# Kernel tuning notes

Hardware: AMD Instinct MI355X
Metric: run time of the kernel (lower is better)

The kernel has to match this reference:

```python
import jax, jax.numpy as jnp
import numpy as np

K_TOP = 8
TEMP = 1.0
GUMBEL_EPS = 1e-20
GEN_EPS = 1e-7
NEG_INF = -1e9


def _genconv(xn, src, dst, e, We, be, W1, b1, W2, b2):
    """GENConv: edge-proj, m=relu(x_src+e)+eps, per-dst softmax aggregation (t=1),
    residual add, then 2-layer MLP."""
    N = xn.shape[0]
    ep = e @ We + be                         # [E, C]
    m = jax.nn.relu(xn[src] + ep) + GEN_EPS  # [E, C]
    mx = jax.ops.segment_max(m, dst, num_segments=N)
    mx = jnp.where(jnp.isfinite(mx), mx, 0.0)
    w = jnp.exp(m - mx[dst])
    den = jax.ops.segment_sum(w, dst, num_segments=N)
    agg = jax.ops.segment_sum(w * m, dst, num_segments=N) / jnp.where(den > 0, den, 1.0)
    out = agg + xn
    return jax.nn.relu(out @ W1 + b1) @ W2 + b2


def setup_inputs() -> dict:
    key = jax.random.key(0)
    ks = jax.random.split(key, 16)
    N, E, D, ED = 1024, 16384, 128, 16
    H1, H2, OUT = 64, 64, 40
    s = 0.02
    return {
        "x": jax.random.normal(ks[0], (N, D), jnp.float32),
        "edge_attr": jax.random.normal(ks[1], (E, ED), jnp.float32),
        "gumbel_u": jax.random.uniform(ks[2], (N, N), jnp.float32),
        "mlp_w": jax.random.normal(ks[3], (ED + 2 * D, 1), jnp.float32) * s,
        "mlp_b": jnp.zeros((1,), jnp.float32),
        "c1_we": jax.random.normal(ks[4], (ED, D), jnp.float32) * s,
        "c1_be": jnp.zeros((D,), jnp.float32),
        "c1_w1": jax.random.normal(ks[5], (D, 2 * D), jnp.float32) * s,
        "c1_b1": jnp.zeros((2 * D,), jnp.float32),
        "c1_w2": jax.random.normal(ks[6], (2 * D, H1), jnp.float32) * s,
        "c1_b2": jnp.zeros((H1,), jnp.float32),
        "c2_we": jax.random.normal(ks[7], (ED, H1), jnp.float32) * s,
        "c2_be": jnp.zeros((H1,), jnp.float32),
        "c2_w1": jax.random.normal(ks[8], (H1, 2 * H1), jnp.float32) * s,
        "c2_b1": jnp.zeros((2 * H1,), jnp.float32),
        "c2_w2": jax.random.normal(ks[9], (2 * H1, H2), jnp.float32) * s,
        "c2_b2": jnp.zeros((H2,), jnp.float32),
        "fc_w": jax.random.normal(ks[10], (H2, OUT), jnp.float32) * s,
        "fc_b": jnp.zeros((OUT,), jnp.float32),
        "num_nodes": N,
        "edge_index": jax.random.randint(ks[11], (2, E), 0, N),
        "node_mask": jnp.ones((N,), jnp.int32),
    }


def reference(x, edge_attr, gumbel_u, mlp_w, mlp_b,
              c1_we, c1_be, c1_w1, c1_b1, c1_w2, c1_b2,
              c2_we, c2_be, c2_w1, c2_b1, c2_w2, c2_b2,
              fc_w, fc_b, num_nodes, edge_index, node_mask):
    N, D = x.shape
    src, dst = edge_index[0], edge_index[1]

    # dense adjacency (duplicate edges sum, only used as a zero/nonzero mask)
    adj = jnp.zeros((N, N), x.dtype).at[src, dst].add(1.0)

    # Edge-score MLP on concat([x_u, x_v*mask, edge_attr_dense]) decomposed
    # linearly (same math as scoring the dense [N,N,2D+ED] feature tensor).
    w_node, w_nb, w_e = mlp_w[:D], mlp_w[D:2 * D], mlp_w[2 * D:]
    s_edge = jnp.zeros((N, N), x.dtype).at[src, dst].set((edge_attr @ w_e)[:, 0])
    score = (x @ w_node) + (x @ w_nb).T * (adj > 0) + s_edge + mlp_b[0]
    score = jnp.where(adj == 0, NEG_INF, score)

    z = jax.nn.softmax(score, axis=-1)
    g = -jnp.log(-jnp.log(gumbel_u + GUMBEL_EPS) + GUMBEL_EPS)
    z = jax.nn.softmax((z + g) / TEMP, axis=-1)

    # top-k edge sampling; softmax output is strictly positive so valid_mask
    # (z>0) is always all-True and shapes stay static at N*k edges.
    _, topi = jax.lax.top_k(z, K_TOP)                       # [N, k]
    new_src = jnp.repeat(jnp.arange(N), K_TOP)
    new_dst = topi.reshape(-1)

    # match each new edge against old edge list (argmax of boolean equality,
    # unmatched edges fall back to index 0 exactly as torch argmax does)
    eq = (edge_index[0][None, :] == new_src[:, None]) & \
         (edge_index[1][None, :] == new_dst[:, None])       # [N*k, E]
    new_attr = edge_attr[jnp.argmax(eq, axis=-1)]

    h = _genconv(x, new_src, new_dst, new_attr, c1_we, c1_be, c1_w1, c1_b1, c1_w2, c1_b2)
    h = jax.nn.relu(h)
    h = _genconv(h, new_src, new_dst, new_attr, c2_we, c2_be, c2_w1, c2_b1, c2_w2, c2_b2)
    h = jax.nn.relu(h)
    out = h @ fc_w + fc_b
    # node_mask is all ones, so x[node_mask != 0] == identity; masked write
    # keeps static shapes under jit.
    return jnp.where((node_mask != 0)[:, None], out, 0.0)
```

## Files before the change

### kernel.cpp

```cpp
#include <hip/hip_runtime.h>
#include <cfloat>

#define NN   1024
#define NE   16384
#define D0   128
#define EDIM 16
#define NH1  64
#define NOUT 40
#define KTOP 8
#define NEGINF (-1000000000.0f)

#define OFF_IDMAX   0u
#define OFF_IDMIN   4194304u
#define OFF_MX1     8388608u
#define OFF_DEN1    8912896u
#define OFF_NUM1    9437184u
#define OFF_MX2     9961472u
#define OFF_DEN2    10223616u
#define OFF_NUM2    10485760u
#define ZERO_LEN    2359296u
#define OFF_A       10747904u
#define OFF_B       10752000u
#define OFF_DST     10756096u
#define OFF_EM      10788864u
#define OFF_M1      10821632u
#define OFF_OUT1    15015936u
#define OFF_T1      15540224u
#define OFF_H       16588800u
#define OFF_M2      16850944u
#define OFF_OUT2    18948096u
#define OFF_T2      19210240u

__global__ __launch_bounds__(256) void scatter_kernel(
    const int* __restrict__ ei, int* __restrict__ idmax, unsigned* __restrict__ idmin)
{
    int e = blockIdx.x * 256 + threadIdx.x;
    if (e >= NE) return;
    int s = ei[e];
    int d = ei[NE + e];
    int idx = s * NN + d;
    atomicMax(idmax + idx, e);
    atomicMin(idmin + idx, (unsigned)e);
}

__global__ __launch_bounds__(256) void ab_kernel(
    const float* __restrict__ x, const float* __restrict__ mlp_w,
    float* __restrict__ a, float* __restrict__ b)
{
    int i = blockIdx.x * 256 + threadIdx.x;
    if (i >= NN) return;
    const float* xr = x + i * D0;
    float sa = 0.f, sb = 0.f;
    for (int d = 0; d < D0; d++) {
        float xv = xr[d];
        sa += xv * mlp_w[d];
        sb += xv * mlp_w[D0 + d];
    }
    a[i] = sa;
    b[i] = sb;
}

__global__ __launch_bounds__(256) void row_topk_kernel(
    const int* __restrict__ idmax, const unsigned* __restrict__ idmin,
    const float* __restrict__ ea, const float* __restrict__ mlp_w,
    const float* __restrict__ mlp_b, const float* __restrict__ a,
    const float* __restrict__ b, const float* __restrict__ u,
    int* __restrict__ dsti, int* __restrict__ ematch)
{
    __shared__ float sv[NN];
    __shared__ float red_v[256];
    __shared__ int   red_j[256];
    const int i = blockIdx.x;
    const int t = threadIdx.x;
    const int rowoff = i * NN;
    const float bias = mlp_b[0];
    const float ai = a[i];
    float we[EDIM];
    #pragma unroll
    for (int k = 0; k < EDIM; k++) we[k] = mlp_w[2 * D0 + k];

    float lmax = NEGINF;
    for (int j = t; j < NN; j += 256) {
        int id = idmax[rowoff + j];
        float s;
        if (id >= 0) {
            const float* er = ea + id * EDIM;
            float se = 0.f;
            #pragma unroll
            for (int k = 0; k < EDIM; k++) se += er[k] * we[k];
            s = ((ai + b[j]) + se) + bias;
        } else {
            s = NEGINF;
        }
        sv[j] = s;
        lmax = fmaxf(lmax, s);
    }
    red_v[t] = lmax;
    __syncthreads();
    for (int stp = 128; stp > 0; stp >>= 1) {
        if (t < stp) red_v[t] = fmaxf(red_v[t], red_v[t + stp]);
        __syncthreads();
    }
    float rowmax = red_v[0];
    __syncthreads();
    bool noedge = (rowmax == NEGINF);

    float lsum = 0.f;
    for (int j = t; j < NN; j += 256) {
        float e;
        if (noedge) e = 1.0f;
        else {
            float s = sv[j];
            e = (s == NEGINF) ? 0.0f : expf(s - rowmax);
        }
        sv[j] = e;
        lsum += e;
    }
    __syncthreads();
    red_v[t] = lsum;
    __syncthreads();
    for (int stp = 128; stp > 0; stp >>= 1) {
        if (t < stp) red_v[t] += red_v[t + stp];
        __syncthreads();
    }
    float rsum = red_v[0];
    __syncthreads();

    for (int j = t; j < NN; j += 256) {
        float z = sv[j] / rsum;
        float uu = u[rowoff + j];
        float g = -logf(-logf(uu + 1e-20f) + 1e-20f);
        sv[j] = z + g;
    }
    __syncthreads();

    for (int sel = 0; sel < KTOP; sel++) {
        float bv = -FLT_MAX;
        int bj = NN;
        for (int j = t; j < NN; j += 256) {
            float v = sv[j];
            if (v > bv || (v == bv && j < bj)) { bv = v; bj = j; }
        }
        red_v[t] = bv; red_j[t] = bj;
        __syncthreads();
        for (int stp = 128; stp > 0; stp >>= 1) {
            if (t < stp) {
                float ov = red_v[t + stp]; int oj = red_j[t + stp];
                if (ov > red_v[t] || (ov == red_v[t] && oj < red_j[t])) {
                    red_v[t] = ov; red_j[t] = oj;
                }
            }
            __syncthreads();
        }
        if (t == 0) {
            int j = red_j[0];
            dsti[i * KTOP + sel] = j;
            unsigned em = idmin[rowoff + j];
            ematch[i * KTOP + sel] = (em == 0xFFFFFFFFu) ? 0 : (int)em;
            sv[j] = -FLT_MAX;
        }
        __syncthreads();
    }
}

template<int Dd>
__global__ __launch_bounds__(256) void genconv_m_kernel(
    const float* __restrict__ xin, const float* __restrict__ ea,
    const float* __restrict__ we, const float* __restrict__ be,
    const int* __restrict__ ematch, const int* __restrict__ dsti,
    float* __restrict__ m, float* __restrict__ mx)
{
    int gid = blockIdx.x * 256 + threadIdx.x;
    int n = gid / Dd;
    int d = gid % Dd;
    int i = n >> 3;
    int e = ematch[n];
    const float* er = ea + e * EDIM;
    float ep = 0.f;
    #pragma unroll
    for (int k = 0; k < EDIM; k++) ep += er[k] * we[k * Dd + d];
    ep += be[d];
    float v = xin[i * Dd + d] + ep;
    float mm = fmaxf(v, 0.f) + 1e-7f;
    m[n * Dd + d] = mm;
    int dst = dsti[n];
    atomicMax((int*)(mx + dst * Dd + d), __float_as_int(mm));
}

template<int Dd>
__global__ __launch_bounds__(256) void genconv_w_kernel(
    const float* __restrict__ m, const float* __restrict__ mx,
    const int* __restrict__ dsti, float* __restrict__ den, float* __restrict__ num)
{
    int gid = blockIdx.x * 256 + threadIdx.x;
    int n = gid / Dd;
    int d = gid % Dd;
    int dst = dsti[n];
    float mm = m[n * Dd + d];
    float w = expf(mm - mx[dst * Dd + d]);
    atomicAdd(den + dst * Dd + d, w);
    atomicAdd(num + dst * Dd + d, w * mm);
}

template<int Dd>
__global__ __launch_bounds__(256) void genconv_agg_kernel(
    const float* __restrict__ num, const float* __restrict__ den,
    const float* __restrict__ xin, float* __restrict__ out)
{
    int gid = blockIdx.x * 256 + threadIdx.x;
    float dn = den[gid];
    float agg = num[gid] / (dn > 0.f ? dn : 1.f);
    out[gid] = agg + xin[gid];
}

template<int Din, int Dout, bool RELU>
__global__ __launch_bounds__(Dout) void mlp_kernel(
    const float* __restrict__ A, const float* __restrict__ W,
    const float* __restrict__ bias, float* __restrict__ C)
{
    __shared__ float arow[Din];
    int r = blockIdx.x, t = threadIdx.x;
    for (int d = t; d < Din; d += Dout) arow[d] = A[r * Din + d];
    __syncthreads();
    float acc = 0.f;
    for (int d = 0; d < Din; d++) acc += arow[d] * W[d * Dout + t];
    acc += bias[t];
    if (RELU) acc = fmaxf(acc, 0.f);
    C[r * Dout + t] = acc;
}

__global__ __launch_bounds__(64) void final_kernel(
    const float* __restrict__ t2, const float* __restrict__ w2,
    const float* __restrict__ b2, const float* __restrict__ fcw,
    const float* __restrict__ fcb, const int* __restrict__ mask,
    float* __restrict__ out)
{
    __shared__ float arow[2 * NH1];
    __shared__ float h2[NH1];
    int r = blockIdx.x, t = threadIdx.x;
    for (int d = t; d < 2 * NH1; d += 64) arow[d] = t2[r * 2 * NH1 + d];
    __syncthreads();
    float acc = 0.f;
    for (int d = 0; d < 2 * NH1; d++) acc += arow[d] * w2[d * NH1 + t];
    acc += b2[t];
    h2[t] = fmaxf(acc, 0.f);
    __syncthreads();
    if (t < NOUT) {
        float o = 0.f;
        for (int d = 0; d < NH1; d++) o += h2[d] * fcw[d * NOUT + t];
        o += fcb[t];
        out[r * NOUT + t] = (mask[r] != 0) ? o : 0.f;
    }
}

extern "C" void kernel_launch(void* const* d_in, const int* in_sizes, int n_in,
                              void* d_out, int out_size, void* d_ws, size_t ws_size,
                              hipStream_t stream) {
    const float* x      = (const float*)d_in[0];
    const float* ea     = (const float*)d_in[1];
    const float* u      = (const float*)d_in[2];
    const float* mlp_w  = (const float*)d_in[3];
    const float* mlp_b  = (const float*)d_in[4];
    const float* c1_we  = (const float*)d_in[5];
    const float* c1_be  = (const float*)d_in[6];
    const float* c1_w1  = (const float*)d_in[7];
    const float* c1_b1  = (const float*)d_in[8];
    const float* c1_w2  = (const float*)d_in[9];
    const float* c1_b2  = (const float*)d_in[10];
    const float* c2_we  = (const float*)d_in[11];
    const float* c2_be  = (const float*)d_in[12];
    const float* c2_w1  = (const float*)d_in[13];
    const float* c2_b1  = (const float*)d_in[14];
    const float* c2_w2  = (const float*)d_in[15];
    const float* c2_b2  = (const float*)d_in[16];
    const float* fc_w   = (const float*)d_in[17];
    const float* fc_b   = (const float*)d_in[18];
    const int*   ei     = (const int*)d_in[20];
    const int*   mask   = (const int*)d_in[21];

    char* ws = (char*)d_ws;
    int*      idmax = (int*)(ws + OFF_IDMAX);
    unsigned* idmin = (unsigned*)(ws + OFF_IDMIN);
    float* mx1  = (float*)(ws + OFF_MX1);
    float* den1 = (float*)(ws + OFF_DEN1);
    float* num1 = (float*)(ws + OFF_NUM1);
    float* mx2  = (float*)(ws + OFF_MX2);
    float* den2 = (float*)(ws + OFF_DEN2);
    float* num2 = (float*)(ws + OFF_NUM2);
    float* a    = (float*)(ws + OFF_A);
    float* b    = (float*)(ws + OFF_B);
    int*   dsti = (int*)(ws + OFF_DST);
    int*   em   = (int*)(ws + OFF_EM);
    float* m1   = (float*)(ws + OFF_M1);
    float* out1 = (float*)(ws + OFF_OUT1);
    float* t1   = (float*)(ws + OFF_T1);
    float* h    = (float*)(ws + OFF_H);
    float* m2   = (float*)(ws + OFF_M2);
    float* out2 = (float*)(ws + OFF_OUT2);
    float* t2   = (float*)(ws + OFF_T2);
    float* out  = (float*)d_out;

    hipMemsetAsync(ws + OFF_IDMAX, 0xFF, 2u * 4194304u, stream);
    hipMemsetAsync(ws + OFF_MX1, 0, ZERO_LEN, stream);

    scatter_kernel<<<(NE + 255) / 256, 256, 0, stream>>>(ei, idmax, idmin);
    ab_kernel<<<(NN + 255) / 256, 256, 0, stream>>>(x, mlp_w, a, b);
    row_topk_kernel<<<NN, 256, 0, stream>>>(idmax, idmin, ea, mlp_w, mlp_b, a, b, u, dsti, em);

    genconv_m_kernel<D0><<<(NN * KTOP * D0) / 256, 256, 0, stream>>>(x, ea, c1_we, c1_be, em, dsti, m1, mx1);
    genconv_w_kernel<D0><<<(NN * KTOP * D0) / 256, 256, 0, stream>>>(m1, mx1, dsti, den1, num1);
    genconv_agg_kernel<D0><<<(NN * D0) / 256, 256, 0, stream>>>(num1, den1, x, out1);
    mlp_kernel<128, 256, true><<<NN, 256, 0, stream>>>(out1, c1_w1, c1_b1, t1);
    mlp_kernel<256, 64, true><<<NN, 64, 0, stream>>>(t1, c1_w2, c1_b2, h);

    genconv_m_kernel<NH1><<<(NN * KTOP * NH1) / 256, 256, 0, stream>>>(h, ea, c2_we, c2_be, em, dsti, m2, mx2);
    genconv_w_kernel<NH1><<<(NN * KTOP * NH1) / 256, 256, 0, stream>>>(m2, mx2, dsti, den2, num2);
    genconv_agg_kernel<NH1><<<(NN * NH1) / 256, 256, 0, stream>>>(num2, den2, h, out2);
    mlp_kernel<64, 128, true><<<NN, 128, 0, stream>>>(out2, c2_w1, c2_b1, t2);

    final_kernel<<<NN, 64, 0, stream>>>(t2, c2_w2, c2_b2, fc_w, fc_b, mask, out);
}
```

Before: 187.0 us.

## Fuse pipeline into four kernels with per-row edge scan and dst-gather aggregation

Drops the 8MB dense edge-id matrices and their memsets. Each top-k block now scans the full edge list for its own source row and builds max/min edge ids in shared memory. GENConv aggregation switches from atomic scatter to a per-destination gather: each block collects its incoming edges, sorts them, and fuses softmax aggregation with both MLP layers (and the final FC for layer 2). Block reductions move to wave shuffles and launch count drops sharply. The cost is redundant scanning (every block reads all 16K edges or all 8K dsti entries), and in-degree is capped at 256, which could truncate heavily loaded destinations.

```diff
diff --git a/kernel.cpp b/kernel.cpp
--- a/kernel.cpp
+++ b/kernel.cpp
@@ -10,84 +10,69 @@
 #define KTOP 8
 #define NEGINF (-1000000000.0f)
 
-#define OFF_IDMAX   0u
-#define OFF_IDMIN   4194304u
-#define OFF_MX1     8388608u
-#define OFF_DEN1    8912896u
-#define OFF_NUM1    9437184u
-#define OFF_MX2     9961472u
-#define OFF_DEN2    10223616u
-#define OFF_NUM2    10485760u
-#define ZERO_LEN    2359296u
-#define OFF_A       10747904u
-#define OFF_B       10752000u
-#define OFF_DST     10756096u
-#define OFF_EM      10788864u
-#define OFF_M1      10821632u
-#define OFF_OUT1    15015936u
-#define OFF_T1      15540224u
-#define OFF_H       16588800u
-#define OFF_M2      16850944u
-#define OFF_OUT2    18948096u
-#define OFF_T2      19210240u
-
-__global__ __launch_bounds__(256) void scatter_kernel(
-    const int* __restrict__ ei, int* __restrict__ idmax, unsigned* __restrict__ idmin)
-{
-    int e = blockIdx.x * 256 + threadIdx.x;
-    if (e >= NE) return;
-    int s = ei[e];
-    int d = ei[NE + e];
-    int idx = s * NN + d;
-    atomicMax(idmax + idx, e);
-    atomicMin(idmin + idx, (unsigned)e);
+#define OFF_A    0u
+#define OFF_B    4096u
+#define OFF_DST  8192u
+#define OFF_EM   40960u
+#define OFF_H    73728u
+
+__device__ __forceinline__ void amx(float& v, int& j, float ov, int oj) {
+    if (ov > v || (ov == v && oj < j)) { v = ov; j = oj; }
 }
 
 __global__ __launch_bounds__(256) void ab_kernel(
     const float* __restrict__ x, const float* __restrict__ mlp_w,
     float* __restrict__ a, float* __restrict__ b)
 {
-    int i = blockIdx.x * 256 + threadIdx.x;
-    if (i >= NN) return;
-    const float* xr = x + i * D0;
-    float sa = 0.f, sb = 0.f;
-    for (int d = 0; d < D0; d++) {
-        float xv = xr[d];
-        sa += xv * mlp_w[d];
-        sb += xv * mlp_w[D0 + d];
-    }
-    a[i] = sa;
-    b[i] = sb;
+    int t = threadIdx.x, lane = t & 63, wid = t >> 6;
+    int row = blockIdx.x * 4 + wid;
+    const float* xr = x + row * D0;
+    float x0 = xr[lane], x1 = xr[64 + lane];
+    float sa = x0 * mlp_w[lane]       + x1 * mlp_w[64 + lane];
+    float sb = x0 * mlp_w[128 + lane] + x1 * mlp_w[192 + lane];
+    for (int s = 32; s; s >>= 1) { sa += __shfl_down(sa, s); sb += __shfl_down(sb, s); }
+    if (lane == 0) { a[row] = sa; b[row] = sb; }
 }
 
 __global__ __launch_bounds__(256) void row_topk_kernel(
-    const int* __restrict__ idmax, const unsigned* __restrict__ idmin,
     const float* __restrict__ ea, const float* __restrict__ mlp_w,
     const float* __restrict__ mlp_b, const float* __restrict__ a,
     const float* __restrict__ b, const float* __restrict__ u,
-    int* __restrict__ dsti, int* __restrict__ ematch)
+    const int* __restrict__ ei, int* __restrict__ dsti, int* __restrict__ em)
 {
     __shared__ float sv[NN];
-    __shared__ float red_v[256];
-    __shared__ int   red_j[256];
-    const int i = blockIdx.x;
-    const int t = threadIdx.x;
-    const int rowoff = i * NN;
-    const float bias = mlp_b[0];
-    const float ai = a[i];
+    __shared__ int   idmx[NN];
+    __shared__ int   idmn[NN];
+    __shared__ float wred[4];
+    __shared__ int   wredj[4];
+    const int i = blockIdx.x, t = threadIdx.x;
+    const int lane = t & 63, wid = t >> 6;
+
+    for (int j = t; j < NN; j += 256) { idmx[j] = -1; idmn[j] = 0x7FFFFFFF; }
+    __syncthreads();
+    for (int e = t; e < NE; e += 256) {
+        if (ei[e] == i) {
+            int dj = ei[NE + e];
+            atomicMax(&idmx[dj], e);
+            atomicMin(&idmn[dj], e);
+        }
+    }
+    __syncthreads();
+
     float we[EDIM];
     #pragma unroll
     for (int k = 0; k < EDIM; k++) we[k] = mlp_w[2 * D0 + k];
+    const float bias = mlp_b[0];
+    const float ai = a[i];
 
     float lmax = NEGINF;
     for (int j = t; j < NN; j += 256) {
-        int id = idmax[rowoff + j];
+        int id = idmx[j];
         float s;
         if (id >= 0) {
-            const float* er = ea + id * EDIM;
             float se = 0.f;
             #pragma unroll
-            for (int k = 0; k < EDIM; k++) se += er[k] * we[k];
+            for (int k = 0; k < EDIM; k++) se += ea[id * EDIM + k] * we[k];
             s = ((ai + b[j]) + se) + bias;
         } else {
             s = NEGINF;
@@ -95,161 +80,215 @@
         sv[j] = s;
         lmax = fmaxf(lmax, s);
     }
-    red_v[t] = lmax;
-    __syncthreads();
-    for (int stp = 128; stp > 0; stp >>= 1) {
-        if (t < stp) red_v[t] = fmaxf(red_v[t], red_v[t + stp]);
-        __syncthreads();
-    }
-    float rowmax = red_v[0];
-    __syncthreads();
+    for (int s = 32; s; s >>= 1) lmax = fmaxf(lmax, __shfl_down(lmax, s));
+    if (lane == 0) wred[wid] = lmax;
+    __syncthreads();
+    float rowmax = fmaxf(fmaxf(wred[0], wred[1]), fmaxf(wred[2], wred[3]));
     bool noedge = (rowmax == NEGINF);
+    __syncthreads();
 
     float lsum = 0.f;
     for (int j = t; j < NN; j += 256) {
-        float e;
-        if (noedge) e = 1.0f;
-        else {
-            float s = sv[j];
-            e = (s == NEGINF) ? 0.0f : expf(s - rowmax);
-        }
-        sv[j] = e;
-        lsum += e;
-    }
-    __syncthreads();
-    red_v[t] = lsum;
-    __syncthreads();
-    for (int stp = 128; stp > 0; stp >>= 1) {
-        if (t < stp) red_v[t] += red_v[t + stp];
-        __syncthreads();
-    }
-    float rsum = red_v[0];
+        float evv;
+        if (noedge) evv = 1.0f;
+        else { float s = sv[j]; evv = (s == NEGINF) ? 0.0f : expf(s - rowmax); }
+        sv[j] = evv;
+        lsum += evv;
+    }
+    for (int s = 32; s; s >>= 1) lsum += __shfl_down(lsum, s);
+    if (lane == 0) wred[wid] = lsum;
+    __syncthreads();
+    float rsum = wred[0] + wred[1] + wred[2] + wred[3];
     __syncthreads();
 
     for (int j = t; j < NN; j += 256) {
         float z = sv[j] / rsum;
-        float uu = u[rowoff + j];
+        float uu = u[i * NN + j];
         float g = -logf(-logf(uu + 1e-20f) + 1e-20f);
         sv[j] = z + g;
     }
     __syncthreads();
 
     for (int sel = 0; sel < KTOP; sel++) {
-        float bv = -FLT_MAX;
-        int bj = NN;
-        for (int j = t; j < NN; j += 256) {
-            float v = sv[j];
-            if (v > bv || (v == bv && j < bj)) { bv = v; bj = j; }
-        }
-        red_v[t] = bv; red_j[t] = bj;
+        float bv = -FLT_MAX; int bj = NN;
+        for (int j = t; j < NN; j += 256) amx(bv, bj, sv[j], j);
+        for (int s = 32; s; s >>= 1) {
+            float ov = __shfl_down(bv, s); int oj = __shfl_down(bj, s);
+            amx(bv, bj, ov, oj);
+        }
+        if (lane == 0) { wred[wid] = bv; wredj[wid] = bj; }
         __syncthreads();
-        for (int stp = 128; stp > 0; stp >>= 1) {
-            if (t < stp) {
-                float ov = red_v[t + stp]; int oj = red_j[t + stp];
-                if (ov > red_v[t] || (ov == red_v[t] && oj < red_j[t])) {
-                    red_v[t] = ov; red_j[t] = oj;
-                }
-            }
-            __syncthreads();
-        }
         if (t == 0) {
-            int j = red_j[0];
+            float v = wred[0]; int j = wredj[0];
+            amx(v, j, wred[1], wredj[1]);
+            amx(v, j, wred[2], wredj[2]);
+            amx(v, j, wred[3], wredj[3]);
             dsti[i * KTOP + sel] = j;
-            unsigned em = idmin[rowoff + j];
-            ematch[i * KTOP + sel] = (em == 0xFFFFFFFFu) ? 0 : (int)em;
+            int mn = idmn[j];
+            em[i * KTOP + sel] = (mn == 0x7FFFFFFF) ? 0 : mn;
             sv[j] = -FLT_MAX;
         }
         __syncthreads();
     }
 }
 
-template<int Dd>
-__global__ __launch_bounds__(256) void genconv_m_kernel(
-    const float* __restrict__ xin, const float* __restrict__ ea,
-    const float* __restrict__ we, const float* __restrict__ be,
-    const int* __restrict__ ematch, const int* __restrict__ dsti,
-    float* __restrict__ m, float* __restrict__ mx)
+__global__ __launch_bounds__(128) void genconv1_kernel(
+    const float* __restrict__ x, const float* __restrict__ ea,
+    const float* __restrict__ we_g, const float* __restrict__ be,
+    const float* __restrict__ w1, const float* __restrict__ b1,
+    const float* __restrict__ w2, const float* __restrict__ b2,
+    const int* __restrict__ dsti, const int* __restrict__ em,
+    float* __restrict__ h)
 {
-    int gid = blockIdx.x * 256 + threadIdx.x;
-    int n = gid / Dd;
-    int d = gid % Dd;
-    int i = n >> 3;
-    int e = ematch[n];
-    const float* er = ea + e * EDIM;
-    float ep = 0.f;
+    __shared__ int   slots[256];
+    __shared__ float eatt[256 * EDIM];
+    __shared__ float arow[D0];
+    __shared__ float t1[2 * D0];
+    __shared__ int   lcnt;
+    const int r = blockIdx.x, t = threadIdx.x;
+    if (t == 0) lcnt = 0;
+    __syncthreads();
+    for (int n = t; n < NN * KTOP; n += 128)
+        if (dsti[n] == r) { int p = atomicAdd(&lcnt, 1); if (p < 256) slots[p] = n; }
+    __syncthreads();
+    int cnt = min(lcnt, 256);
+    if (t == 0) {
+        for (int p = 1; p < cnt; p++) {
+            int v = slots[p]; int q = p - 1;
+            while (q >= 0 && slots[q] > v) { slots[q + 1] = slots[q]; q--; }
+            slots[q + 1] = v;
+        }
+    }
+    __syncthreads();
+    for (int q = t; q < cnt * EDIM; q += 128)
+        eatt[q] = ea[em[slots[q >> 4]] * EDIM + (q & 15)];
+    __syncthreads();
+
+    const int d = t;
+    float wed[EDIM];
     #pragma unroll
-    for (int k = 0; k < EDIM; k++) ep += er[k] * we[k * Dd + d];
-    ep += be[d];
-    float v = xin[i * Dd + d] + ep;
-    float mm = fmaxf(v, 0.f) + 1e-7f;
-    m[n * Dd + d] = mm;
-    int dst = dsti[n];
-    atomicMax((int*)(mx + dst * Dd + d), __float_as_int(mm));
-}
-
-template<int Dd>
-__global__ __launch_bounds__(256) void genconv_w_kernel(
-    const float* __restrict__ m, const float* __restrict__ mx,
-    const int* __restrict__ dsti, float* __restrict__ den, float* __restrict__ num)
+    for (int k = 0; k < EDIM; k++) wed[k] = we_g[k * D0 + d];
+    const float bed = be[d];
+
+    float mxv = -FLT_MAX;
+    for (int idx = 0; idx < cnt; idx++) {
+        int n = slots[idx]; int src = n >> 3;
+        float ep = bed;
+        #pragma unroll
+        for (int k = 0; k < EDIM; k++) ep += eatt[idx * EDIM + k] * wed[k];
+        float m = fmaxf(x[src * D0 + d] + ep, 0.f) + 1e-7f;
+        mxv = fmaxf(mxv, m);
+    }
+    float den = 0.f, num = 0.f;
+    for (int idx = 0; idx < cnt; idx++) {
+        int n = slots[idx]; int src = n >> 3;
+        float ep = bed;
+        #pragma unroll
+        for (int k = 0; k < EDIM; k++) ep += eatt[idx * EDIM + k] * wed[k];
+        float m = fmaxf(x[src * D0 + d] + ep, 0.f) + 1e-7f;
+        float w = expf(m - mxv);
+        den += w; num += w * m;
+    }
+    float agg = cnt ? num / (den > 0.f ? den : 1.f) : 0.f;
+    arow[d] = agg + x[r * D0 + d];
+    __syncthreads();
+
+    float acc0 = b1[d], acc1 = b1[d + D0];
+    for (int k = 0; k < D0; k++) {
+        float av = arow[k];
+        acc0 += av * w1[k * 2 * D0 + d];
+        acc1 += av * w1[k * 2 * D0 + d + D0];
+    }
+    t1[d] = fmaxf(acc0, 0.f);
+    t1[d + D0] = fmaxf(acc1, 0.f);
+    __syncthreads();
+    if (t < NH1) {
+        float acc = b2[t];
+        for (int k = 0; k < 2 * D0; k++) acc += t1[k] * w2[k * NH1 + t];
+        h[r * NH1 + t] = fmaxf(acc, 0.f);
+    }
+}
+
+__global__ __launch_bounds__(128) void genconv2_kernel(
+    const float* __restrict__ h, const float* __restrict__ ea,
+    const float* __restrict__ we_g, const float* __restrict__ be,
+    const float* __restrict__ w1, const float* __restrict__ b1,
+    const float* __restrict__ w2, const float* __restrict__ b2,
+    const float* __restrict__ fcw, const float* __restrict__ fcb,
+    const int* __restrict__ dsti, const int* __restrict__ em,
+    const int* __restrict__ mask, float* __restrict__ out)
 {
-    int gid = blockIdx.x * 256 + threadIdx.x;
-    int n = gid / Dd;
-    int d = gid % Dd;
-    int dst = dsti[n];
-    float mm = m[n * Dd + d];
-    float w = expf(mm - mx[dst * Dd + d]);
-    atomicAdd(den + dst * Dd + d, w);
-    atomicAdd(num + dst * Dd + d, w * mm);
-}
-
-template<int Dd>
-__global__ __launch_bounds__(256) void genconv_agg_kernel(
-    const float* __restrict__ num, const float* __restrict__ den,
-    const float* __restrict__ xin, float* __restrict__ out)
-{
-    int gid = blockIdx.x * 256 + threadIdx.x;
-    float dn = den[gid];
-    float agg = num[gid] / (dn > 0.f ? dn : 1.f);
-    out[gid] = agg + xin[gid];
-}
-
-template<int Din, int Dout, bool RELU>
-__global__ __launch_bounds__(Dout) void mlp_kernel(
-    const float* __restrict__ A, const float* __restrict__ W,
-    const float* __restrict__ bias, float* __restrict__ C)
-{
-    __shared__ float arow[Din];
-    int r = blockIdx.x, t = threadIdx.x;
-    for (int d = t; d < Din; d += Dout) arow[d] = A[r * Din + d];
-    __syncthreads();
-    float acc = 0.f;
-    for (int d = 0; d < Din; d++) acc += arow[d] * W[d * Dout + t];
-    acc += bias[t];
-    if (RELU) acc = fmaxf(acc, 0.f);
-    C[r * Dout + t] = acc;
-}
-
-__global__ __launch_bounds__(64) void final_kernel(
-    const float* __restrict__ t2, const float* __restrict__ w2,
-    const float* __restrict__ b2, const float* __restrict__ fcw,
-    const float* __restrict__ fcb, const int* __restrict__ mask,
-    float* __restrict__ out)
-{
-    __shared__ float arow[2 * NH1];
+    __shared__ int   slots[256];
+    __shared__ float eatt[256 * EDIM];
+    __shared__ float arow[NH1];
+    __shared__ float t2[2 * NH1];
     __shared__ float h2[NH1];
-    int r = blockIdx.x, t = threadIdx.x;
-    for (int d = t; d < 2 * NH1; d += 64) arow[d] = t2[r * 2 * NH1 + d];
-    __syncthreads();
-    float acc = 0.f;
-    for (int d = 0; d < 2 * NH1; d++) acc += arow[d] * w2[d * NH1 + t];
-    acc += b2[t];
-    h2[t] = fmaxf(acc, 0.f);
+    __shared__ int   lcnt;
+    const int r = blockIdx.x, t = threadIdx.x;
+    if (t == 0) lcnt = 0;
+    __syncthreads();
+    for (int n = t; n < NN * KTOP; n += 128)
+        if (dsti[n] == r) { int p = atomicAdd(&lcnt, 1); if (p < 256) slots[p] = n; }
+    __syncthreads();
+    int cnt = min(lcnt, 256);
+    if (t == 0) {
+        for (int p = 1; p < cnt; p++) {
+            int v = slots[p]; int q = p - 1;
+            while (q >= 0 && slots[q] > v) { slots[q + 1] = slots[q]; q--; }
+            slots[q + 1] = v;
+        }
+    }
+    __syncthreads();
+    for (int q = t; q < cnt * EDIM; q += 128)
+        eatt[q] = ea[em[slots[q >> 4]] * EDIM + (q & 15)];
+    __syncthreads();
+
+    if (t < NH1) {
+        const int d = t;
+        float wed[EDIM];
+        #pragma unroll
+        for (int k = 0; k < EDIM; k++) wed[k] = we_g[k * NH1 + d];
+        const float bed = be[d];
+        float mxv = -FLT_MAX;
+        for (int idx = 0; idx < cnt; idx++) {
+            int n = slots[idx]; int src = n >> 3;
+            float ep = bed;
+            #pragma unroll
+            for (int k = 0; k < EDIM; k++) ep += eatt[idx * EDIM + k] * wed[k];
+            float m = fmaxf(h[src * NH1 + d] + ep, 0.f) + 1e-7f;
+            mxv = fmaxf(mxv, m);
+        }
+        float den = 0.f, num = 0.f;
+        for (int idx = 0; idx < cnt; idx++) {
+            int n = slots[idx]; int src = n >> 3;
+            float ep = bed;
+            #pragma unroll
+            for (int k = 0; k < EDIM; k++) ep += eatt[idx * EDIM + k] * wed[k];
+            float m = fmaxf(h[src * NH1 + d] + ep, 0.f) + 1e-7f;
+            float w = expf(m - mxv);
+            den += w; num += w * m;
+        }
+        float agg = cnt ? num / (den > 0.f ? den : 1.f) : 0.f;
+        arow[d] = agg + h[r * NH1 + d];
+    }
+    __syncthreads();
+
+    {
+        float acc = b1[t];
+        for (int k = 0; k < NH1; k++) acc += arow[k] * w1[k * 2 * NH1 + t];
+        t2[t] = fmaxf(acc, 0.f);
+    }
+    __syncthreads();
+    if (t < NH1) {
+        float acc = b2[t];
+        for (int k = 0; k < 2 * NH1; k++) acc += t2[k] * w2[k * NH1 + t];
+        h2[t] = fmaxf(acc, 0.f);
+    }
     __syncthreads();
     if (t < NOUT) {
-        float o = 0.f;
-        for (int d = 0; d < NH1; d++) o += h2[d] * fcw[d * NOUT + t];
-        o += fcb[t];
-        out[r * NOUT + t] = (mask[r] != 0) ? o : 0.f;
+        float acc = fcb[t];
+        for (int k = 0; k < NH1; k++) acc += h2[k] * fcw[k * NOUT + t];
+        out[r * NOUT + t] = (mask[r] != 0) ? acc : 0.f;
     }
 }
 
@@ -279,44 +318,17 @@
     const int*   mask   = (const int*)d_in[21];
 
     char* ws = (char*)d_ws;
-    int*      idmax = (int*)(ws + OFF_IDMAX);
-    unsigned* idmin = (unsigned*)(ws + OFF_IDMIN);
-    float* mx1  = (float*)(ws + OFF_MX1);
-    float* den1 = (float*)(ws + OFF_DEN1);
-    float* num1 = (float*)(ws + OFF_NUM1);
-    float* mx2  = (float*)(ws + OFF_MX2);
-    float* den2 = (float*)(ws + OFF_DEN2);
-    float* num2 = (float*)(ws + OFF_NUM2);
     float* a    = (float*)(ws + OFF_A);
     float* b    = (float*)(ws + OFF_B);
     int*   dsti = (int*)(ws + OFF_DST);
     int*   em   = (int*)(ws + OFF_EM);
-    float* m1   = (float*)(ws + OFF_M1);
-    float* out1 = (float*)(ws + OFF_OUT1);
-    float* t1   = (float*)(ws + OFF_T1);
     float* h    = (float*)(ws + OFF_H);
-    float* m2   = (float*)(ws + OFF_M2);
-    float* out2 = (float*)(ws + OFF_OUT2);
-    float* t2   = (float*)(ws + OFF_T2);
     float* out  = (float*)d_out;
 
-    hipMemsetAsync(ws + OFF_IDMAX, 0xFF, 2u * 4194304u, stream);
-    hipMemsetAsync(ws + OFF_MX1, 0, ZERO_LEN, stream);
-
-    scatter_kernel<<<(NE + 255) / 256, 256, 0, stream>>>(ei, idmax, idmin);
-    ab_kernel<<<(NN + 255) / 256, 256, 0, stream>>>(x, mlp_w, a, b);
-    row_topk_kernel<<<NN, 256, 0, stream>>>(idmax, idmin, ea, mlp_w, mlp_b, a, b, u, dsti, em);
-
-    genconv_m_kernel<D0><<<(NN * KTOP * D0) / 256, 256, 0, stream>>>(x, ea, c1_we, c1_be, em, dsti, m1, mx1);
-    genconv_w_kernel<D0><<<(NN * KTOP * D0) / 256, 256, 0, stream>>>(m1, mx1, dsti, den1, num1);
-    genconv_agg_kernel<D0><<<(NN * D0) / 256, 256, 0, stream>>>(num1, den1, x, out1);
-    mlp_kernel<128, 256, true><<<NN, 256, 0, stream>>>(out1, c1_w1, c1_b1, t1);
-    mlp_kernel<256, 64, true><<<NN, 64, 0, stream>>>(t1, c1_w2, c1_b2, h);
-
-    genconv_m_kernel<NH1><<<(NN * KTOP * NH1) / 256, 256, 0, stream>>>(h, ea, c2_we, c2_be, em, dsti, m2, mx2);
-    genconv_w_kernel<NH1><<<(NN * KTOP * NH1) / 256, 256, 0, stream>>>(m2, mx2, dsti, den2, num2);
-    genconv_agg_kernel<NH1><<<(NN * NH1) / 256, 256, 0, stream>>>(num2, den2, h, out2);
-    mlp_kernel<64, 128, true><<<NN, 128, 0, stream>>>(out2, c2_w1, c2_b1, t2);
-
-    final_kernel<<<NN, 64, 0, stream>>>(t2, c2_w2, c2_b2, fc_w, fc_b, mask, out);
-}
+    ab_kernel<<<NN / 4, 256, 0, stream>>>(x, mlp_w, a, b);
+    row_topk_kernel<<<NN, 256, 0, stream>>>(ea, mlp_w, mlp_b, a, b, u, ei, dsti, em);
+    genconv1_kernel<<<NN, 128, 0, stream>>>(x, ea, c1_we, c1_be, c1_w1, c1_b1, c1_w2, c1_b2,
+                                            dsti, em, h);
+    genconv2_kernel<<<NN, 128, 0, stream>>>(h, ea, c2_we, c2_be, c2_w1, c2_b1, c2_w2, c2_b2,
+                                            fc_w, fc_b, dsti, em, mask, out);
+}
```

Measured after the change: 192.0 us. 2.7% more time.
